# Optimization experiments

Measured on AMD Instinct MI355X. Metric: run time of the kernel, lower is better.

Reference implementation:

```python
import jax, jax.numpy as jnp
import numpy as np

N = 50000      # nodes
E = 1_600_000  # edges
IN, H, H2, OUT = 256, 128, 64, 2
EPS = 1e-5     # BatchNorm eps


def setup_inputs() -> dict:
    key = jax.random.key(0)
    ks = jax.random.split(key, 18)
    inp = {
        "x": jax.random.normal(ks[0], (N, IN), dtype=jnp.float32),
        "edge_index": jax.random.randint(ks[1], (2, E), 0, N, dtype=jnp.int64),
        # GCNConv 1
        "W1": jax.random.normal(ks[2], (IN, H), dtype=jnp.float32) / np.sqrt(IN),
        "b1": jnp.zeros((H,), dtype=jnp.float32),
        "g1": jnp.ones((H,), dtype=jnp.float32),
        "be1": jnp.zeros((H,), dtype=jnp.float32),
        "m1": jax.random.normal(ks[3], (H,), dtype=jnp.float32) * 0.1,
        "v1": jax.random.uniform(ks[4], (H,), dtype=jnp.float32, minval=0.5, maxval=1.5),
        # GCNConv 2
        "W2": jax.random.normal(ks[5], (H, H2), dtype=jnp.float32) / np.sqrt(H),
        "b2": jnp.zeros((H2,), dtype=jnp.float32),
        "g2": jnp.ones((H2,), dtype=jnp.float32),
        "be2": jnp.zeros((H2,), dtype=jnp.float32),
        "m2": jax.random.normal(ks[6], (H2,), dtype=jnp.float32) * 0.1,
        "v2": jax.random.uniform(ks[7], (H2,), dtype=jnp.float32, minval=0.5, maxval=1.5),
        # final linear
        "Wl": jax.random.normal(ks[8], (H2, OUT), dtype=jnp.float32) / np.sqrt(H2),
        "bl": jnp.zeros((OUT,), dtype=jnp.float32),
    }
    return inp


def _gcn_conv(x, W, b, src, dst, n_nodes):
    # PyG GCNConv: linear transform, then symmetric-normalized aggregation
    # with self-loops (gcn_norm, improved=False, fill_value=1).
    xw = x @ W                                            # [N, H]
    ones = jnp.ones((src.shape[0],), dtype=x.dtype)
    deg = jax.ops.segment_sum(ones, dst, num_segments=n_nodes) + 1.0  # +1 self-loop
    dinv = jax.lax.rsqrt(deg)                             # deg^{-1/2}
    norm = dinv[src] * dinv[dst]                          # [E]
    msgs = xw[src] * norm[:, None]                        # [E, H] gather
    agg = jax.ops.segment_sum(msgs, dst, num_segments=n_nodes)  # scatter-add
    agg = agg + xw * (1.0 / deg)[:, None]                 # self-loop term
    return agg + b


def _bn_relu(x, gamma, beta, mean, var):
    # inference-mode BatchNorm1d + ReLU
    xhat = (x - mean) * jax.lax.rsqrt(var + EPS)
    return jax.nn.relu(xhat * gamma + beta)


def reference(x, edge_index, W1, b1, g1, be1, m1, v1,
              W2, b2, g2, be2, m2, v2, Wl, bl):
    src, dst = edge_index[0], edge_index[1]
    h = _gcn_conv(x, W1, b1, src, dst, N)
    h = _bn_relu(h, g1, be1, m1, v1)
    # dropout is identity in eval mode
    h = _gcn_conv(h, W2, b2, src, dst, N)
    h = _bn_relu(h, g2, be2, m2, v2)
    return h @ Wl + bl
```

## Files before the change

### kernel.cpp

```cpp
#include <hip/hip_runtime.h>

#define N_NODES 50000
#define N_EDGES 1600000
#define IN_F 256
#define H1_F 128
#define H2_F 64
#define OUT_F 2
#define BN_EPS 1e-5f

#define NBUK 782
#define BCAP 3584
#define CHUNK 4096
#define NCHUNK 391

typedef __attribute__((ext_vector_type(8))) short bf16x8;
typedef __attribute__((ext_vector_type(4))) float f32x4;
typedef __attribute__((ext_vector_type(4))) int   i32x4;
typedef __attribute__((ext_vector_type(4))) unsigned u32x4;

__device__ __forceinline__ unsigned short f2b(float f) {
    union { float f; unsigned u; } v; v.f = f;
    unsigned r = (v.u + 0x7FFFu + ((v.u >> 16) & 1u)) >> 16;
    return (unsigned short)r;
}
__device__ __forceinline__ float b2f(unsigned short b) {
    union { unsigned u; float f; } v; v.u = ((unsigned)b) << 16;
    return v.f;
}
__device__ __forceinline__ void add2(float& a0, float& a1, unsigned u) {
    union { unsigned u; float f; } lo, hi;
    lo.u = u << 16;
    hi.u = u & 0xFFFF0000u;
    a0 += lo.f; a1 += hi.f;
}

__launch_bounds__(256)
__global__ void chist_prep_kernel(const int* __restrict__ dst, int* __restrict__ h,
                                  int* __restrict__ tot,
                                  const float* __restrict__ W1, const float* __restrict__ W2,
                                  unsigned short* __restrict__ w1t, unsigned short* __restrict__ w2t,
                                  const float* __restrict__ g1, const float* __restrict__ be1,
                                  const float* __restrict__ m1, const float* __restrict__ v1,
                                  const float* __restrict__ b1,
                                  const float* __restrict__ g2, const float* __restrict__ be2,
                                  const float* __restrict__ m2, const float* __restrict__ v2,
                                  const float* __restrict__ b2,
                                  float* __restrict__ sc1, float* __restrict__ sh1,
                                  float* __restrict__ sc2, float* __restrict__ sh2) {
    const int blk = blockIdx.x;
    const int t   = threadIdx.x;
    if (blk < NCHUNK) {
        __shared__ int lh[NBUK];
        const int c = blk;
        for (int i = t; i < NBUK; i += 256) lh[i] = 0;
        __syncthreads();
        const int e0 = c * CHUNK;
        const int e1 = min(e0 + CHUNK, N_EDGES);
        const i32x4* p = (const i32x4*)(dst + e0);
        const int n4 = (e1 - e0) >> 2;
        for (int i = t; i < n4; i += 256) {
            i32x4 d = __builtin_nontemporal_load(p + i);
            atomicAdd(&lh[d.x >> 6], 1);
            atomicAdd(&lh[d.y >> 6], 1);
            atomicAdd(&lh[d.z >> 6], 1);
            atomicAdd(&lh[d.w >> 6], 1);
        }
        __syncthreads();
        for (int i = t; i < NBUK; i += 256) {
            int v = lh[i];
            h[(size_t)i * NCHUNK + c] = v;
            if (v) atomicAdd(&tot[i], v);
        }
    } else {
        const int blk2 = blk - NCHUNK;
        if (blk2 < 128) {
            int i = blk2 * 256 + t;
            int n = i / IN_F, k = i % IN_F;
            w1t[i] = f2b(W1[(size_t)k * H1_F + n]);
        } else if (blk2 < 160) {
            int i = (blk2 - 128) * 256 + t;
            int n = i / H1_F, k = i % H1_F;
            w2t[i] = f2b(W2[(size_t)k * H2_F + n]);
        } else {
            if (t < H1_F) {
                float s = g1[t] * rsqrtf(v1[t] + BN_EPS);
                sc1[t] = s;
                sh1[t] = (b1[t] - m1[t]) * s + be1[t];
            } else if (t < H1_F + H2_F) {
                int f = t - H1_F;
                float s = g2[f] * rsqrtf(v2[f] + BN_EPS);
                sc2[f] = s;
                sh2[f] = (b2[f] - m2[f]) * s + be2[f];
            }
        }
    }
}

__launch_bounds__(256)
__global__ void scanoffs_kernel(const int* __restrict__ tot, int* __restrict__ boff,
                                int* __restrict__ h, int* __restrict__ rowptr) {
    const int b = (blockIdx.x * blockDim.x + threadIdx.x) >> 6;
    if (b >= NBUK) return;
    const int lane = threadIdx.x & 63;

    int acc = 0;
    for (int i = lane; i < NBUK; i += 64)
        if (i < b) acc += tot[i];
#pragma unroll
    for (int off = 1; off < 64; off <<= 1) acc += __shfl_xor(acc, off);
    if (lane == 0) boff[b] = acc;
    if (b == 0 && lane == 0) { boff[NBUK] = N_EDGES; rowptr[N_NODES] = N_EDGES; }

    int run = acc;
    int* row = h + (size_t)b * NCHUNK;
    for (int c0 = 0; c0 < NCHUNK; c0 += 64) {
        int idx = c0 + lane;
        int v = (idx < NCHUNK) ? row[idx] : 0;
        int s = v;
#pragma unroll
        for (int off = 1; off < 64; off <<= 1) {
            int t2 = __shfl_up(s, off);
            if (lane >= off) s += t2;
        }
        if (idx < NCHUNK) row[idx] = run + (s - v);
        run += __shfl(s, 63);
    }
}

__launch_bounds__(256)
__global__ void cscatter_kernel(const int* __restrict__ src, const int* __restrict__ dst,
                                const int* __restrict__ h, unsigned* __restrict__ bedges) {
    __shared__ int cur[NBUK];
    const int c = blockIdx.x;
    for (int i = threadIdx.x; i < NBUK; i += 256) cur[i] = h[(size_t)i * NCHUNK + c];
    __syncthreads();
    const int e0 = c * CHUNK;
    const int e1 = min(e0 + CHUNK, N_EDGES);
    const i32x4* pd = (const i32x4*)(dst + e0);
    const i32x4* ps = (const i32x4*)(src + e0);
    const int n4 = (e1 - e0) >> 2;
    for (int i = threadIdx.x; i < n4; i += 256) {
        i32x4 d = __builtin_nontemporal_load(pd + i);
        i32x4 s = __builtin_nontemporal_load(ps + i);
        int slot;
        slot = atomicAdd(&cur[d.x >> 6], 1); bedges[slot] = (unsigned)s.x | ((unsigned)d.x << 16);
        slot = atomicAdd(&cur[d.y >> 6], 1); bedges[slot] = (unsigned)s.y | ((unsigned)d.y << 16);
        slot = atomicAdd(&cur[d.z >> 6], 1); bedges[slot] = (unsigned)s.z | ((unsigned)d.z << 16);
        slot = atomicAdd(&cur[d.w >> 6], 1); bedges[slot] = (unsigned)s.w | ((unsigned)d.w << 16);
    }
}

__launch_bounds__(256)
__global__ void build_kernel(const unsigned* __restrict__ bedges, const int* __restrict__ boff,
                             unsigned short* __restrict__ perm, int* __restrict__ rowptr,
                             float* __restrict__ dinv) {
    __shared__ unsigned e_lds[BCAP];
    __shared__ unsigned short p_lds[BCAP];
    __shared__ int ncnt[64], ncur[64];

    const int b = blockIdx.x;
    const int t = threadIdx.x;
    const int start = boff[b];
    const int end   = boff[b + 1];
    const int cnt   = end - start;
    const bool fits = (cnt <= BCAP);

    if (t < 64) ncnt[t] = 0;
    __syncthreads();

    for (int i = t; i < cnt; i += 256) {
        unsigned e = bedges[start + i];
        if (fits) e_lds[i] = e;
        atomicAdd(&ncnt[(e >> 16) & 63], 1);
    }
    __syncthreads();

    if (t == 0) {
        int a = 0;
        for (int i = 0; i < 64; ++i) { ncur[i] = a; a += ncnt[i]; }
    }
    __syncthreads();

    if (t < 64) {
        int node = b * 64 + t;
        if (node < N_NODES) {
            rowptr[node] = start + ncur[t];
            dinv[node]   = rsqrtf((float)ncnt[t] + 1.0f);
        }
    }
    __syncthreads();

    for (int i = t; i < cnt; i += 256) {
        unsigned e = fits ? e_lds[i] : bedges[start + i];
        int slot = atomicAdd(&ncur[(e >> 16) & 63], 1);
        unsigned short s = (unsigned short)(e & 0xFFFFu);
        if (fits) p_lds[slot] = s;
        else      perm[start + slot] = s;
    }
    if (fits) {
        __syncthreads();
        for (int i = t; i < cnt; i += 256) perm[start + i] = p_lds[i];
    }
}

template <int KSTEPS, int NTILES, bool A_BF16>
__launch_bounds__(256)
__global__ void mfma_gemm_kernel(const void* __restrict__ Ap, const unsigned short* __restrict__ BT,
                                 const float* __restrict__ dscale, unsigned short* __restrict__ C,
                                 int M) {
    constexpr int K  = KSTEPS * 32;
    constexpr int NF = NTILES * 16;
    const int wave = threadIdx.x >> 6;
    const int lane = threadIdx.x & 63;
    const int r0   = (blockIdx.x * 4 + wave) * 16;
    const int m    = lane & 15;
    const int kb   = lane >> 4;

    int arow = r0 + m;
    if (arow >= M) arow = M - 1;

    f32x4 acc[NTILES];
#pragma unroll
    for (int nt = 0; nt < NTILES; ++nt) acc[nt] = (f32x4)(0.f);

#pragma unroll
    for (int ks = 0; ks < KSTEPS; ++ks) {
        const int k0 = ks * 32 + kb * 8;
        bf16x8 a;
        if constexpr (A_BF16) {
            a = *(const bf16x8*)((const unsigned short*)Ap + (size_t)arow * K + k0);
        } else {
            const float* af = (const float*)Ap + (size_t)arow * K + k0;
            f32x4 lo = __builtin_nontemporal_load((const f32x4*)af);
            f32x4 hi = __builtin_nontemporal_load((const f32x4*)(af + 4));
            union { bf16x8 v; unsigned short u[8]; } pk;
            pk.u[0] = f2b(lo.x); pk.u[1] = f2b(lo.y); pk.u[2] = f2b(lo.z); pk.u[3] = f2b(lo.w);
            pk.u[4] = f2b(hi.x); pk.u[5] = f2b(hi.y); pk.u[6] = f2b(hi.z); pk.u[7] = f2b(hi.w);
            a = pk.v;
        }
#pragma unroll
        for (int nt = 0; nt < NTILES; ++nt) {
            bf16x8 b = *(const bf16x8*)(BT + (size_t)(nt * 16 + m) * K + k0);
            acc[nt] = __builtin_amdgcn_mfma_f32_16x16x32_bf16(a, b, acc[nt], 0, 0, 0);
        }
    }

#pragma unroll
    for (int reg = 0; reg < 4; ++reg) {
        const int r = r0 + kb * 4 + reg;
        if (r < M) {
            const float ds = dscale[r];
#pragma unroll
            for (int nt = 0; nt < NTILES; ++nt)
                C[(size_t)r * NF + nt * 16 + m] = f2b(acc[nt][reg] * ds);
        }
    }
}

template <int HF, bool FINAL>
__launch_bounds__(256)
__global__ void agg_kernel(const int* __restrict__ rowptr, const unsigned short* __restrict__ perm,
                           const unsigned short* __restrict__ xw, const float* __restrict__ dinv,
                           const float* __restrict__ sc, const float* __restrict__ sh,
                           const float* __restrict__ Wl, const float* __restrict__ bl,
                           void* __restrict__ outp) {
    constexpr int LPE = HF / 8;
    constexpr int G   = 64 / LPE;
    const int wave = threadIdx.x >> 6;
    const int node = blockIdx.x * 4 + wave;
    if (node >= N_NODES) return;
    const int lane = threadIdx.x & 63;
    const int grp  = lane / LPE;
    const int fl   = (lane % LPE) * 8;

    float aA[8];
#pragma unroll
    for (int i = 0; i < 8; ++i) aA[i] = 0.f;

    if (grp == 0) {
        u32x4 u = *(const u32x4*)(xw + (size_t)node * HF + fl);
#pragma unroll
        for (int i = 0; i < 4; ++i) add2(aA[2 * i], aA[2 * i + 1], u[i]);
    }

    const int start = rowptr[node];
    const int end   = rowptr[node + 1];
    for (int base = start; base < end; base += 64) {
        int pidx = base + lane;
        int pv = (int)__builtin_nontemporal_load(perm + (pidx < end ? pidx : end - 1));
        int ne = end - base;
        if (ne > 64) ne = 64;
        if (ne == 64) {
#pragma unroll
            for (int j = 0; j < 64; j += G) {
                int s = __shfl(pv, j + grp);
                u32x4 u = *(const u32x4*)(xw + (size_t)s * HF + fl);
#pragma unroll
                for (int i = 0; i < 4; ++i) add2(aA[2 * i], aA[2 * i + 1], u[i]);
            }
        } else {
            for (int j = 0; j < ne; j += G) {
                int s = __shfl(pv, j + grp);
                if (j + grp < ne) {
                    u32x4 u = *(const u32x4*)(xw + (size_t)s * HF + fl);
#pragma unroll
                    for (int i = 0; i < 4; ++i) add2(aA[2 * i], aA[2 * i + 1], u[i]);
                }
            }
        }
    }

#pragma unroll
    for (int off = LPE; off < 64; off <<= 1)
#pragma unroll
        for (int i = 0; i < 8; ++i) aA[i] += __shfl_xor(aA[i], off);

    const float dv = dinv[node];
    f32x4 scl = *(const f32x4*)(sc + fl);
    f32x4 sch = *(const f32x4*)(sc + fl + 4);
    f32x4 shl = *(const f32x4*)(sh + fl);
    f32x4 shh = *(const f32x4*)(sh + fl + 4);
    float y[8];
#pragma unroll
    for (int i = 0; i < 4; ++i) {
        y[i]     = fmaxf(aA[i] * (dv * scl[i]) + shl[i], 0.f);
        y[i + 4] = fmaxf(aA[i + 4] * (dv * sch[i]) + shh[i], 0.f);
    }

    if constexpr (!FINAL) {
        if (lane < LPE) {
            u32x4 o;
#pragma unroll
            for (int i = 0; i < 4; ++i)
                o[i] = (unsigned)f2b(y[2 * i]) | ((unsigned)f2b(y[2 * i + 1]) << 16);
            __builtin_nontemporal_store(o, (u32x4*)((unsigned short*)outp + (size_t)node * HF + fl));
        }
    } else {
        float p0 = 0.f, p1 = 0.f;
#pragma unroll
        for (int i = 0; i < 8; ++i) {
            p0 += y[i] * Wl[(fl + i) * 2 + 0];
            p1 += y[i] * Wl[(fl + i) * 2 + 1];
        }
#pragma unroll
        for (int off = 1; off < LPE; off <<= 1) {
            p0 += __shfl_xor(p0, off);
            p1 += __shfl_xor(p1, off);
        }
        if (lane == 0) {
            float* o = (float*)outp;
            o[(size_t)node * 2 + 0] = p0 + bl[0];
            o[(size_t)node * 2 + 1] = p1 + bl[1];
        }
    }
}

extern "C" void kernel_launch(void* const* d_in, const int* in_sizes, int n_in,
                              void* d_out, int out_size, void* d_ws, size_t ws_size,
                              hipStream_t stream) {
    const float* x   = (const float*)d_in[0];
    const int*   ei  = (const int*)d_in[1];
    const float* W1  = (const float*)d_in[2];
    const float* b1  = (const float*)d_in[3];
    const float* g1  = (const float*)d_in[4];
    const float* be1 = (const float*)d_in[5];
    const float* m1  = (const float*)d_in[6];
    const float* v1  = (const float*)d_in[7];
    const float* W2  = (const float*)d_in[8];
    const float* b2  = (const float*)d_in[9];
    const float* g2  = (const float*)d_in[10];
    const float* be2 = (const float*)d_in[11];
    const float* m2  = (const float*)d_in[12];
    const float* v2  = (const float*)d_in[13];
    const float* Wl  = (const float*)d_in[14];
    const float* bl  = (const float*)d_in[15];

    const int* src = ei;
    const int* dst = ei + N_EDGES;

    int*            h      = (int*)d_ws;
    int*            tot    = h + (size_t)NBUK * NCHUNK;
    int*            boff   = tot + 1024;
    int*            rowptr = boff + 1024;
    float*          dinv   = (float*)(rowptr + 50016);
    float*          sc1    = dinv + 50016;
    float*          sh1    = sc1 + 128;
    float*          sc2    = sh1 + 128;
    float*          sh2    = sc2 + 64;
    unsigned*       bedges = (unsigned*)(sh2 + 64);
    unsigned short* perm   = (unsigned short*)(bedges + N_EDGES);
    unsigned short* xwb    = perm + N_EDGES;
    unsigned short* h1b    = xwb + (size_t)N_NODES * H1_F;
    unsigned short* w1t    = h1b + (size_t)N_NODES * H1_F;
    unsigned short* w2t    = w1t + H1_F * IN_F;

    hipMemsetAsync(tot, 0, 1024 * sizeof(int), stream);

    chist_prep_kernel<<<NCHUNK + 161, 256, 0, stream>>>(dst, h, tot,
                                                        W1, W2, w1t, w2t,
                                                        g1, be1, m1, v1, b1,
                                                        g2, be2, m2, v2, b2,
                                                        sc1, sh1, sc2, sh2);
    scanoffs_kernel<<<(NBUK * 64 + 255) / 256, 256, 0, stream>>>(tot, boff, h, rowptr);
    cscatter_kernel<<<NCHUNK, 256, 0, stream>>>(src, dst, h, bedges);
    build_kernel<<<NBUK, 256, 0, stream>>>(bedges, boff, perm, rowptr, dinv);

    mfma_gemm_kernel<IN_F / 32, H1_F / 16, false><<<(N_NODES + 63) / 64, 256, 0, stream>>>(
        x, w1t, dinv, xwb, N_NODES);
    agg_kernel<H1_F, false><<<(N_NODES + 3) / 4, 256, 0, stream>>>(
        rowptr, perm, xwb, dinv, sc1, sh1, nullptr, nullptr, h1b);

    mfma_gemm_kernel<H1_F / 32, H2_F / 16, true><<<(N_NODES + 63) / 64, 256, 0, stream>>>(
        h1b, w2t, dinv, xwb, N_NODES);
    agg_kernel<H2_F, true><<<(N_NODES + 3) / 4, 256, 0, stream>>>(
        rowptr, perm, xwb, dinv, sc2, sh2, Wl, bl, (float*)d_out);
}
```

Measured before the change: 254.0 us.

## Compute degrees early and co-launch first GEMM with edge scatter kernel

Node degrees are now counted with global atomics during the histogram pass, and dinv is computed in the scan kernel instead of the build kernel. Because dinv is ready earlier, the first MFMA GEMM (x @ W1 scaled by dinv) is merged into the edge-scatter launch as extra blocks, so the compute-bound GEMM can overlap the memory- and atomic-bound scatter and one launch is removed. In exchange the histogram pass issues 1.6M global atomics on the deg array, and the deg buffer has to be zeroed by a larger memset.

```diff
diff --git a/kernel.cpp b/kernel.cpp
--- a/kernel.cpp
+++ b/kernel.cpp
@@ -36,7 +36,7 @@
 
 __launch_bounds__(256)
 __global__ void chist_prep_kernel(const int* __restrict__ dst, int* __restrict__ h,
-                                  int* __restrict__ tot,
+                                  int* __restrict__ tot, int* __restrict__ deg,
                                   const float* __restrict__ W1, const float* __restrict__ W2,
                                   unsigned short* __restrict__ w1t, unsigned short* __restrict__ w2t,
                                   const float* __restrict__ g1, const float* __restrict__ be1,
@@ -64,6 +64,10 @@
             atomicAdd(&lh[d.y >> 6], 1);
             atomicAdd(&lh[d.z >> 6], 1);
             atomicAdd(&lh[d.w >> 6], 1);
+            atomicAdd(&deg[d.x], 1);
+            atomicAdd(&deg[d.y], 1);
+            atomicAdd(&deg[d.z], 1);
+            atomicAdd(&deg[d.w], 1);
         }
         __syncthreads();
         for (int i = t; i < NBUK; i += 256) {
@@ -98,10 +102,14 @@
 
 __launch_bounds__(256)
 __global__ void scanoffs_kernel(const int* __restrict__ tot, int* __restrict__ boff,
-                                int* __restrict__ h, int* __restrict__ rowptr) {
+                                int* __restrict__ h, int* __restrict__ rowptr,
+                                const int* __restrict__ deg, float* __restrict__ dinv) {
     const int b = (blockIdx.x * blockDim.x + threadIdx.x) >> 6;
     if (b >= NBUK) return;
     const int lane = threadIdx.x & 63;
+
+    const int node = b * 64 + lane;
+    if (node < N_NODES) dinv[node] = rsqrtf((float)deg[node] + 1.0f);
 
     int acc = 0;
     for (int i = lane; i < NBUK; i += 64)
@@ -128,32 +136,82 @@
 }
 
 __launch_bounds__(256)
-__global__ void cscatter_kernel(const int* __restrict__ src, const int* __restrict__ dst,
-                                const int* __restrict__ h, unsigned* __restrict__ bedges) {
+__global__ void cscatter_gemm1_kernel(const int* __restrict__ src, const int* __restrict__ dst,
+                                      const int* __restrict__ h, unsigned* __restrict__ bedges,
+                                      const float* __restrict__ x, const unsigned short* __restrict__ BT,
+                                      const float* __restrict__ dinv, unsigned short* __restrict__ C) {
     __shared__ int cur[NBUK];
-    const int c = blockIdx.x;
-    for (int i = threadIdx.x; i < NBUK; i += 256) cur[i] = h[(size_t)i * NCHUNK + c];
-    __syncthreads();
-    const int e0 = c * CHUNK;
-    const int e1 = min(e0 + CHUNK, N_EDGES);
-    const i32x4* pd = (const i32x4*)(dst + e0);
-    const i32x4* ps = (const i32x4*)(src + e0);
-    const int n4 = (e1 - e0) >> 2;
-    for (int i = threadIdx.x; i < n4; i += 256) {
-        i32x4 d = __builtin_nontemporal_load(pd + i);
-        i32x4 s = __builtin_nontemporal_load(ps + i);
-        int slot;
-        slot = atomicAdd(&cur[d.x >> 6], 1); bedges[slot] = (unsigned)s.x | ((unsigned)d.x << 16);
-        slot = atomicAdd(&cur[d.y >> 6], 1); bedges[slot] = (unsigned)s.y | ((unsigned)d.y << 16);
-        slot = atomicAdd(&cur[d.z >> 6], 1); bedges[slot] = (unsigned)s.z | ((unsigned)d.z << 16);
-        slot = atomicAdd(&cur[d.w >> 6], 1); bedges[slot] = (unsigned)s.w | ((unsigned)d.w << 16);
+    const int blk = blockIdx.x;
+    if (blk < NCHUNK) {
+        const int c = blk;
+        for (int i = threadIdx.x; i < NBUK; i += 256) cur[i] = h[(size_t)i * NCHUNK + c];
+        __syncthreads();
+        const int e0 = c * CHUNK;
+        const int e1 = min(e0 + CHUNK, N_EDGES);
+        const i32x4* pd = (const i32x4*)(dst + e0);
+        const i32x4* ps = (const i32x4*)(src + e0);
+        const int n4 = (e1 - e0) >> 2;
+        for (int i = threadIdx.x; i < n4; i += 256) {
+            i32x4 d = __builtin_nontemporal_load(pd + i);
+            i32x4 s = __builtin_nontemporal_load(ps + i);
+            int slot;
+            slot = atomicAdd(&cur[d.x >> 6], 1); bedges[slot] = (unsigned)s.x | ((unsigned)d.x << 16);
+            slot = atomicAdd(&cur[d.y >> 6], 1); bedges[slot] = (unsigned)s.y | ((unsigned)d.y << 16);
+            slot = atomicAdd(&cur[d.z >> 6], 1); bedges[slot] = (unsigned)s.z | ((unsigned)d.z << 16);
+            slot = atomicAdd(&cur[d.w >> 6], 1); bedges[slot] = (unsigned)s.w | ((unsigned)d.w << 16);
+        }
+    } else {
+        constexpr int KSTEPS = IN_F / 32;
+        constexpr int NTILES = H1_F / 16;
+        constexpr int K  = IN_F;
+        constexpr int NF = H1_F;
+        const int bid2 = blk - NCHUNK;
+        const int wave = threadIdx.x >> 6;
+        const int lane = threadIdx.x & 63;
+        const int r0   = (bid2 * 4 + wave) * 16;
+        const int m    = lane & 15;
+        const int kb   = lane >> 4;
+
+        int arow = r0 + m;
+        if (arow >= N_NODES) arow = N_NODES - 1;
+
+        f32x4 acc[NTILES];
+#pragma unroll
+        for (int nt = 0; nt < NTILES; ++nt) acc[nt] = (f32x4)(0.f);
+
+#pragma unroll
+        for (int ks = 0; ks < KSTEPS; ++ks) {
+            const int k0 = ks * 32 + kb * 8;
+            const float* af = x + (size_t)arow * K + k0;
+            f32x4 lo = __builtin_nontemporal_load((const f32x4*)af);
+            f32x4 hi = __builtin_nontemporal_load((const f32x4*)(af + 4));
+            union { bf16x8 v; unsigned short u[8]; } pk;
+            pk.u[0] = f2b(lo.x); pk.u[1] = f2b(lo.y); pk.u[2] = f2b(lo.z); pk.u[3] = f2b(lo.w);
+            pk.u[4] = f2b(hi.x); pk.u[5] = f2b(hi.y); pk.u[6] = f2b(hi.z); pk.u[7] = f2b(hi.w);
+            bf16x8 a = pk.v;
+#pragma unroll
+            for (int nt = 0; nt < NTILES; ++nt) {
+                bf16x8 b = *(const bf16x8*)(BT + (size_t)(nt * 16 + m) * K + k0);
+                acc[nt] = __builtin_amdgcn_mfma_f32_16x16x32_bf16(a, b, acc[nt], 0, 0, 0);
+            }
+        }
+
+#pragma unroll
+        for (int reg = 0; reg < 4; ++reg) {
+            const int r = r0 + kb * 4 + reg;
+            if (r < N_NODES) {
+                const float ds = dinv[r];
+#pragma unroll
+                for (int nt = 0; nt < NTILES; ++nt)
+                    C[(size_t)r * NF + nt * 16 + m] = f2b(acc[nt][reg] * ds);
+            }
+        }
     }
 }
 
 __launch_bounds__(256)
 __global__ void build_kernel(const unsigned* __restrict__ bedges, const int* __restrict__ boff,
-                             unsigned short* __restrict__ perm, int* __restrict__ rowptr,
-                             float* __restrict__ dinv) {
+                             unsigned short* __restrict__ perm, int* __restrict__ rowptr) {
     __shared__ unsigned e_lds[BCAP];
     __shared__ unsigned short p_lds[BCAP];
     __shared__ int ncnt[64], ncur[64];
@@ -183,10 +241,7 @@
 
     if (t < 64) {
         int node = b * 64 + t;
-        if (node < N_NODES) {
-            rowptr[node] = start + ncur[t];
-            dinv[node]   = rsqrtf((float)ncnt[t] + 1.0f);
-        }
+        if (node < N_NODES) rowptr[node] = start + ncur[t];
     }
     __syncthreads();
 
@@ -203,11 +258,10 @@
     }
 }
 
-template <int KSTEPS, int NTILES, bool A_BF16>
-__launch_bounds__(256)
-__global__ void mfma_gemm_kernel(const void* __restrict__ Ap, const unsigned short* __restrict__ BT,
-                                 const float* __restrict__ dscale, unsigned short* __restrict__ C,
-                                 int M) {
+template <int KSTEPS, int NTILES>
+__launch_bounds__(256)
+__global__ void mfma_gemm2_kernel(const unsigned short* __restrict__ Ap, const unsigned short* __restrict__ BT,
+                                  const float* __restrict__ dscale, unsigned short* __restrict__ C) {
     constexpr int K  = KSTEPS * 32;
     constexpr int NF = NTILES * 16;
     const int wave = threadIdx.x >> 6;
@@ -217,7 +271,7 @@
     const int kb   = lane >> 4;
 
     int arow = r0 + m;
-    if (arow >= M) arow = M - 1;
+    if (arow >= N_NODES) arow = N_NODES - 1;
 
     f32x4 acc[NTILES];
 #pragma unroll
@@ -226,18 +280,7 @@
 #pragma unroll
     for (int ks = 0; ks < KSTEPS; ++ks) {
         const int k0 = ks * 32 + kb * 8;
-        bf16x8 a;
-        if constexpr (A_BF16) {
-            a = *(const bf16x8*)((const unsigned short*)Ap + (size_t)arow * K + k0);
-        } else {
-            const float* af = (const float*)Ap + (size_t)arow * K + k0;
-            f32x4 lo = __builtin_nontemporal_load((const f32x4*)af);
-            f32x4 hi = __builtin_nontemporal_load((const f32x4*)(af + 4));
-            union { bf16x8 v; unsigned short u[8]; } pk;
-            pk.u[0] = f2b(lo.x); pk.u[1] = f2b(lo.y); pk.u[2] = f2b(lo.z); pk.u[3] = f2b(lo.w);
-            pk.u[4] = f2b(hi.x); pk.u[5] = f2b(hi.y); pk.u[6] = f2b(hi.z); pk.u[7] = f2b(hi.w);
-            a = pk.v;
-        }
+        bf16x8 a = *(const bf16x8*)(Ap + (size_t)arow * K + k0);
 #pragma unroll
         for (int nt = 0; nt < NTILES; ++nt) {
             bf16x8 b = *(const bf16x8*)(BT + (size_t)(nt * 16 + m) * K + k0);
@@ -248,7 +291,7 @@
 #pragma unroll
     for (int reg = 0; reg < 4; ++reg) {
         const int r = r0 + kb * 4 + reg;
-        if (r < M) {
+        if (r < N_NODES) {
             const float ds = dscale[r];
 #pragma unroll
             for (int nt = 0; nt < NTILES; ++nt)
@@ -380,7 +423,8 @@
 
     int*            h      = (int*)d_ws;
     int*            tot    = h + (size_t)NBUK * NCHUNK;
-    int*            boff   = tot + 1024;
+    int*            deg    = tot + 1024;
+    int*            boff   = deg + 50048;
     int*            rowptr = boff + 1024;
     float*          dinv   = (float*)(rowptr + 50016);
     float*          sc1    = dinv + 50016;
@@ -394,24 +438,23 @@
     unsigned short* w1t    = h1b + (size_t)N_NODES * H1_F;
     unsigned short* w2t    = w1t + H1_F * IN_F;
 
-    hipMemsetAsync(tot, 0, 1024 * sizeof(int), stream);
-
-    chist_prep_kernel<<<NCHUNK + 161, 256, 0, stream>>>(dst, h, tot,
+    hipMemsetAsync(tot, 0, (1024 + 50048) * sizeof(int), stream);
+
+    chist_prep_kernel<<<NCHUNK + 161, 256, 0, stream>>>(dst, h, tot, deg,
                                                         W1, W2, w1t, w2t,
                                                         g1, be1, m1, v1, b1,
                                                         g2, be2, m2, v2, b2,
                                                         sc1, sh1, sc2, sh2);
-    scanoffs_kernel<<<(NBUK * 64 + 255) / 256, 256, 0, stream>>>(tot, boff, h, rowptr);
-    cscatter_kernel<<<NCHUNK, 256, 0, stream>>>(src, dst, h, bedges);
-    build_kernel<<<NBUK, 256, 0, stream>>>(bedges, boff, perm, rowptr, dinv);
-
-    mfma_gemm_kernel<IN_F / 32, H1_F / 16, false><<<(N_NODES + 63) / 64, 256, 0, stream>>>(
-        x, w1t, dinv, xwb, N_NODES);
+    scanoffs_kernel<<<(NBUK * 64 + 255) / 256, 256, 0, stream>>>(tot, boff, h, rowptr, deg, dinv);
+    cscatter_gemm1_kernel<<<NCHUNK + (N_NODES + 63) / 64, 256, 0, stream>>>(
+        src, dst, h, bedges, x, w1t, dinv, xwb);
+    build_kernel<<<NBUK, 256, 0, stream>>>(bedges, boff, perm, rowptr);
+
     agg_kernel<H1_F, false><<<(N_NODES + 3) / 4, 256, 0, stream>>>(
         rowptr, perm, xwb, dinv, sc1, sh1, nullptr, nullptr, h1b);
 
-    mfma_gemm_kernel<H1_F / 32, H2_F / 16, true><<<(N_NODES + 63) / 64, 256, 0, stream>>>(
-        h1b, w2t, dinv, xwb, N_NODES);
+    mfma_gemm2_kernel<H1_F / 32, H2_F / 16><<<(N_NODES + 63) / 64, 256, 0, stream>>>(
+        h1b, w2t, dinv, xwb);
     agg_kernel<H2_F, true><<<(N_NODES + 3) / 4, 256, 0, stream>>>(
         rowptr, perm, xwb, dinv, sc2, sh2, Wl, bl, (float*)d_out);
 }
```

Measured after the change: 299.8 us. 1.18x slower.
